# Kernel tuning notes

Measured on AMD Instinct MI355X. Metric: run time of the kernel, lower is better.

## Reference

```python
import jax, jax.numpy as jnp
import numpy as np

L_SIDE = 32
N_PIX = 12 * L_SIDE * L_SIDE      # 12288 sphere pixels
N_VALID = N_PIX // 2              # theta <= pi/2 hemisphere (first half by construction)
A_TH, B_TH, C_TH = 0.03, 1.0, 1.0  # ellipsoid semi-axes (thickness, 1, 1)


def _sphere_angles(n):
    # Deterministic Fibonacci-lattice sphere sampling standing in for SphereHealpix.
    i = np.arange(n, dtype=np.float64)
    z = 1.0 - 2.0 * (i + 0.5) / n          # cos(theta), descending -> theta<=pi/2 iff i < n/2
    theta = np.arccos(z)
    phi = (i * np.pi * (3.0 - np.sqrt(5.0))) % (2.0 * np.pi)
    return theta.astype(np.float32), phi.astype(np.float32)


def _ellipse_valid():
    # Faithful translation of ReconstructionModel.ellipse_valid for the valid hemisphere.
    theta_all, phi_all = _sphere_angles(N_PIX)
    tv = theta_all[:N_VALID].astype(np.float32)
    pv = phi_all[:N_VALID].astype(np.float32)
    a, b, c = np.float32(A_TH), np.float32(B_TH), np.float32(C_TH)
    # cartesian coords of valid pixels (computed BEFORE the angle shift)
    xv = np.cos(pv) * np.sin(tv)
    yv = np.sin(pv) * np.sin(tv)
    # meshgrid(phi, x) / meshgrid(theta, y) with ij indexing -> angles vary on rows, coords on cols
    phi = ((pv + np.pi / 2) % (2 * np.pi)).astype(np.float32)[:, None]   # [Nv,1]
    theta = ((tv + np.pi / 2) % np.pi).astype(np.float32)[:, None]       # [Nv,1]
    x = xv[None, :]
    y = yv[None, :]
    x_c = np.sin(2 * theta) / 2 * np.cos(phi)
    y_c = -np.sin(2 * theta) / 2 * np.sin(phi)
    z_c = (np.cos(2 * theta) + 1) / 2
    r = np.sqrt(2 * (np.cos(2 * theta) + 1)) / 2 + np.float32(1e-5)
    a2, b2, c2 = a * a, b * b, c * c
    ct, st = np.cos(theta), np.sin(theta)
    cp, sp = np.cos(phi), np.sin(phi)
    ct2, ct4 = ct ** 2, ct ** 4
    cp2 = cp ** 2
    x2, y2 = x ** 2, y ** 2
    s2p = np.sin(2.0 * phi)
    with np.errstate(invalid='ignore'):
        S = (-b2 * ct2 + b2 * ct4 - b2 * y2 - c2 * x2
             + a2 * b2 * ct4 + b2 * c2 * ct2 - b2 * c2 * ct4
             - b2 * x2 * cp2 + b2 * y2 * cp2 + c2 * x2 * cp2 - c2 * y2 * cp2
             - a2 * x2 * ct2 + c2 * x2 * ct2
             + b2 * x * y * s2p - c2 * x * y * s2p
             + a2 * x2 * cp2 * ct2 - a2 * y2 * cp2 * ct2
             - c2 * x2 * cp2 * ct2 + c2 * y2 * cp2 * ct2
             + 2.0 * b2 * x * cp * ct * st - 2.0 * b2 * y * ct * sp * st
             + 2.0 * c2 * x * y * cp * ct2 * sp - 2.0 * a2 * x * y * cp * ct2 * sp)
        num = (a * c * np.sqrt(S)
               - a2 * b * ct2 + 2.0 * a2 * b * ct4
               + 2.0 * b * c2 * ct2 - 2.0 * b * c2 * ct4
               + a2 * b * x * cp * ct * st - b * c2 * x * cp * ct * st
               - a2 * b * y * ct * sp * st + b * c2 * y * ct * sp * st)
        den = b * (a2 * ct2 - c2 * ct2 + c2)
        z = num / den
        f = ((x - x_c) ** 2 + (y - y_c) ** 2 + (z - z_c) ** 2) / r ** 2
    f = np.where(np.isnan(f), np.float32(0.0), f)   # f[f != f] = 0
    return f.astype(np.float32)


def setup_inputs() -> dict:
    key = jax.random.key(0)
    x = jax.random.uniform(key, (8, 16, N_PIX), dtype=jnp.float32)
    all_responses = jnp.asarray(_ellipse_valid())   # [N_VALID, N_VALID]
    return {"x": x, "all_responses": all_responses}


def reference(x, all_responses):
    nv = all_responses.shape[0]
    # masked gather: theta <= pi/2 is exactly the first nv pixels by construction
    x_valid = x[:, :, :nv]                                   # [B,C,Nv]
    mixture = jnp.einsum('bcn,nm->bcm', x_valid, all_responses)
    mixture = jnp.clip(mixture, 0.0, 1.0)                    # mix='clip'
    # masked scatter back into zero buffer
    out = jnp.zeros_like(x).at[:, :, :nv].set(mixture)
    return out
```

## Files before the change

kernel.cpp:

```cpp
#include <hip/hip_runtime.h>
#include <hip/hip_bf16.h>


#define NPIX 12288
#define NV   6144
#define MR   128
#define BNW  32
#define KST  128
#define KCH  3072
#define NSI  24

typedef __attribute__((ext_vector_type(8))) short bf16x8;
typedef __attribute__((ext_vector_type(4))) float f32x4;
typedef __attribute__((ext_vector_type(4))) unsigned u32x4;

__device__ __forceinline__ unsigned pk2(float lo, float hi) {
    __hip_bfloat162 h = __float22bfloat162_rn(make_float2(lo, hi));
    union { __hip_bfloat162 h; unsigned u; } v; v.h = h; return v.u;
}

__device__ __forceinline__ bf16x8 cvt8(f32x4 a, f32x4 b) {
    union { unsigned u[4]; bf16x8 v; } r;
    r.u[0] = pk2(a[0], a[1]); r.u[1] = pk2(a[2], a[3]);
    r.u[2] = pk2(b[0], b[1]); r.u[3] = pk2(b[2], b[3]);
    return r.v;
}

__global__ __launch_bounds__(256) void prep_kernel(const float* __restrict__ x,
                                                   unsigned short* __restrict__ abf) {
    int q = blockIdx.x * 256 + threadIdx.x;
    int m = q / (NV / 8);
    int r = q % (NV / 8);
    int k = r * 8;
    const float* src = x + (size_t)m * NPIX + k;
    f32x4 a = *(const f32x4*)(src);
    f32x4 b = *(const f32x4*)(src + 4);
    u32x4 o;
    o[0] = pk2(a[0], a[1]); o[1] = pk2(a[2], a[3]);
    o[2] = pk2(b[0], b[1]); o[3] = pk2(b[2], b[3]);
    *(u32x4*)(abf + (size_t)m * NV + k) = o;
}

__device__ __forceinline__ void sload(const float*& bptr, float2 (&r)[8]) {
    #pragma unroll
    for (int gi = 0; gi < 4; ++gi) {
        const float* p = bptr + (size_t)(gi * 32) * NV;
        r[2 * gi]     = *(const float2*)(p);
        r[2 * gi + 1] = *(const float2*)(p + NV);
    }
    bptr += (size_t)KST * NV;
}

__device__ __forceinline__ void wstage(unsigned char* buf, const float2 (&r)[8],
                                       int kq, int nq, int sw0, int sw1) {
    #pragma unroll
    for (int gi = 0; gi < 4; ++gi) {
        unsigned lo = pk2(r[2 * gi].x, r[2 * gi + 1].x);
        unsigned hi = pk2(r[2 * gi].y, r[2 * gi + 1].y);
        const int kbyte = (kq + gi * 32) * 2;
        *(unsigned*)(buf + nq * 256       + (kbyte ^ sw0)) = lo;
        *(unsigned*)(buf + (nq + 1) * 256 + (kbyte ^ sw1)) = hi;
    }
}

template<bool BF16A>
__device__ __forceinline__ void compute_step(const unsigned char* buf,
        const unsigned short* __restrict__ A, const float* __restrict__ X,
        size_t arow0, size_t arow1, int ln, int lg, f32x4 (&acc)[2][2]) {
    bf16x8 afr[2][4];
    #pragma unroll
    for (int ks = 0; ks < 4; ++ks) {
        if (BF16A) {
            afr[0][ks] = *(const bf16x8*)(A + arow0 + ks * 32);
            afr[1][ks] = *(const bf16x8*)(A + arow1 + ks * 32);
        } else {
            f32x4 p0 = *(const f32x4*)(X + arow0 + ks * 32);
            f32x4 p1 = *(const f32x4*)(X + arow0 + ks * 32 + 4);
            afr[0][ks] = cvt8(p0, p1);
            f32x4 q0 = *(const f32x4*)(X + arow1 + ks * 32);
            f32x4 q1 = *(const f32x4*)(X + arow1 + ks * 32 + 4);
            afr[1][ks] = cvt8(q0, q1);
        }
    }
    const int swn = (ln & 7) << 4;
    #pragma unroll
    for (int nt = 0; nt < 2; ++nt) {
        const int rowb = (nt * 16 + ln) * 256;
        #pragma unroll
        for (int ks = 0; ks < 4; ++ks) {
            bf16x8 bfr = *(const bf16x8*)(buf + rowb + (((lg * 16) + ks * 64) ^ swn));
            acc[0][nt] = __builtin_amdgcn_mfma_f32_16x16x32_bf16(afr[0][ks], bfr, acc[0][nt], 0, 0, 0);
            acc[1][nt] = __builtin_amdgcn_mfma_f32_16x16x32_bf16(afr[1][ks], bfr, acc[1][nt], 0, 0, 0);
        }
    }
}

template<bool BF16A>
__global__ __launch_bounds__(256, 2) void gemm_kernel(const float* __restrict__ X,
        const unsigned short* __restrict__ A, const float* __restrict__ R,
        float* __restrict__ out) {
    __shared__ unsigned char Bs0[32 * 256];
    __shared__ unsigned char Bs1[32 * 256];

    const int tid = threadIdx.x;
    const int w = tid >> 6;
    const int l = tid & 63;
    const int ln = l & 15, lg = l >> 4;
    const int nb = blockIdx.x >> 1, chunk = blockIdx.x & 1;
    const int n0 = nb * BNW;
    const int kbase = chunk * KCH;

    const int kq = (tid >> 4) * 2;
    const int nq = (tid & 15) * 2;
    const float* bptr = R + (size_t)(kbase + kq) * NV + (n0 + nq);
    const int sw0 = (nq & 7) << 4;
    const int sw1 = ((nq + 1) & 7) << 4;

    size_t arow0, arow1;
    if (BF16A) {
        arow0 = (size_t)(w * 32 + ln) * NV + kbase + lg * 8;
        arow1 = arow0 + (size_t)16 * NV;
    } else {
        arow0 = (size_t)(w * 32 + ln) * NPIX + kbase + lg * 8;
        arow1 = arow0 + (size_t)16 * NPIX;
    }

    f32x4 acc[2][2];
    #pragma unroll
    for (int a = 0; a < 2; ++a)
        #pragma unroll
        for (int b = 0; b < 2; ++b) {
            acc[a][b][0] = 0.f; acc[a][b][1] = 0.f;
            acc[a][b][2] = 0.f; acc[a][b][3] = 0.f;
        }

    float2 ring0[8], ring1[8];
    sload(bptr, ring0);
    sload(bptr, ring1);
    wstage(Bs0, ring0, kq, nq, sw0, sw1);
    __syncthreads();

    #pragma unroll 1
    for (int it = 0; it < NSI / 2; ++it) {
        const int s = it * 2;
        if (s + 2 < NSI) sload(bptr, ring0);
        compute_step<BF16A>(Bs0, A, X, arow0, arow1, ln, lg, acc);
        arow0 += KST; arow1 += KST;
        wstage(Bs1, ring1, kq, nq, sw0, sw1);
        __syncthreads();
        if (s + 3 < NSI) sload(bptr, ring1);
        compute_step<BF16A>(Bs1, A, X, arow0, arow1, ln, lg, acc);
        arow0 += KST; arow1 += KST;
        if (s + 2 < NSI) wstage(Bs0, ring0, kq, nq, sw0, sw1);
        __syncthreads();
    }

    #pragma unroll
    for (int mt = 0; mt < 2; ++mt) {
        const int mbase = w * 32 + mt * 16 + lg * 4;
        #pragma unroll
        for (int nt = 0; nt < 2; ++nt) {
            const size_t cb = (size_t)chunk * NV + n0 + nt * 16 + ln;
            #pragma unroll
            for (int j = 0; j < 4; ++j)
                out[(size_t)(mbase + j) * NPIX + cb] = acc[mt][nt][j];
        }
    }
}

__global__ __launch_bounds__(256) void reduce_kernel(float* __restrict__ out) {
    int q = blockIdx.x * 256 + threadIdx.x;
    int m = q / (NV / 4);
    int r = q % (NV / 4);
    size_t base = (size_t)m * NPIX + r * 4;
    f32x4 a = *(f32x4*)(out + base);
    f32x4 b = *(f32x4*)(out + base + NV);
    f32x4 c, z;
    #pragma unroll
    for (int i = 0; i < 4; ++i) {
        float v = a[i] + b[i];
        c[i] = fminf(fmaxf(v, 0.f), 1.f);
        z[i] = 0.f;
    }
    *(f32x4*)(out + base) = c;
    *(f32x4*)(out + base + NV) = z;
}

extern "C" void kernel_launch(void* const* d_in, const int* in_sizes, int n_in,
                              void* d_out, int out_size, void* d_ws, size_t ws_size,
                              hipStream_t stream) {
    const float* x = (const float*)d_in[0];
    const float* R = (const float*)d_in[1];
    float* out = (float*)d_out;

    const bool use_ws = ws_size >= (size_t)MR * NV * 2;
    if (use_ws) {
        unsigned short* abf = (unsigned short*)d_ws;
        prep_kernel<<<(MR * NV / 8) / 256, 256, 0, stream>>>(x, abf);
        gemm_kernel<true><<<(NV / BNW) * 2, 256, 0, stream>>>(x, abf, R, out);
    } else {
        gemm_kernel<false><<<(NV / BNW) * 2, 256, 0, stream>>>(x, nullptr, R, out);
    }
    reduce_kernel<<<(MR * NV / 4) / 256, 256, 0, stream>>>(out);
}
```

Before: 254.4 us.

## Increase split-K chunks to 4 or 8 using workspace partial buffers

Generalizes the split-K GEMM from two K chunks to four or eight, chosen by available workspace. Chunks beyond the first two write partial sums to workspace buffers, and the reduce kernel adds them before clipping. This multiplies the grid from 384 to as many as 1536 blocks so the GPU is better filled. The cost is extra partial-sum writes and reads plus shorter per-block K loops with less pipelining.

```diff
diff --git a/kernel.cpp b/kernel.cpp
--- a/kernel.cpp
+++ b/kernel.cpp
@@ -7,8 +7,8 @@
 #define MR   128
 #define BNW  32
 #define KST  128
-#define KCH  3072
-#define NSI  24
+#define NSTR (NV / BNW)
+#define PARTF ((size_t)MR * NV)
 
 typedef __attribute__((ext_vector_type(8))) short bf16x8;
 typedef __attribute__((ext_vector_type(4))) float f32x4;
@@ -98,7 +98,8 @@
 template<bool BF16A>
 __global__ __launch_bounds__(256, 2) void gemm_kernel(const float* __restrict__ X,
         const unsigned short* __restrict__ A, const float* __restrict__ R,
-        float* __restrict__ out) {
+        float* __restrict__ out, float* __restrict__ wpart,
+        int nchunks, int kch) {
     __shared__ unsigned char Bs0[32 * 256];
     __shared__ unsigned char Bs1[32 * 256];
 
@@ -106,9 +107,11 @@
     const int w = tid >> 6;
     const int l = tid & 63;
     const int ln = l & 15, lg = l >> 4;
-    const int nb = blockIdx.x >> 1, chunk = blockIdx.x & 1;
+    const int chunk = blockIdx.x / NSTR;
+    const int nb = blockIdx.x % NSTR;
     const int n0 = nb * BNW;
-    const int kbase = chunk * KCH;
+    const int kbase = chunk * kch;
+    const int nsi = kch / KST;
 
     const int kq = (tid >> 4) * 2;
     const int nq = (tid & 15) * 2;
@@ -141,48 +144,60 @@
     __syncthreads();
 
     #pragma unroll 1
-    for (int it = 0; it < NSI / 2; ++it) {
+    for (int it = 0; it < nsi / 2; ++it) {
         const int s = it * 2;
-        if (s + 2 < NSI) sload(bptr, ring0);
+        if (s + 2 < nsi) sload(bptr, ring0);
         compute_step<BF16A>(Bs0, A, X, arow0, arow1, ln, lg, acc);
         arow0 += KST; arow1 += KST;
         wstage(Bs1, ring1, kq, nq, sw0, sw1);
         __syncthreads();
-        if (s + 3 < NSI) sload(bptr, ring1);
+        if (s + 3 < nsi) sload(bptr, ring1);
         compute_step<BF16A>(Bs1, A, X, arow0, arow1, ln, lg, acc);
         arow0 += KST; arow1 += KST;
-        if (s + 2 < NSI) wstage(Bs0, ring0, kq, nq, sw0, sw1);
+        if (s + 2 < nsi) wstage(Bs0, ring0, kq, nq, sw0, sw1);
         __syncthreads();
     }
 
+    float* dst;
+    size_t rstride;
+    if (chunk < 2) { dst = out + (size_t)chunk * NV; rstride = NPIX; }
+    else           { dst = wpart + (size_t)(chunk - 2) * PARTF; rstride = NV; }
     #pragma unroll
     for (int mt = 0; mt < 2; ++mt) {
         const int mbase = w * 32 + mt * 16 + lg * 4;
         #pragma unroll
         for (int nt = 0; nt < 2; ++nt) {
-            const size_t cb = (size_t)chunk * NV + n0 + nt * 16 + ln;
+            const size_t cb = (size_t)(n0 + nt * 16 + ln);
             #pragma unroll
             for (int j = 0; j < 4; ++j)
-                out[(size_t)(mbase + j) * NPIX + cb] = acc[mt][nt][j];
-        }
-    }
-}
-
-__global__ __launch_bounds__(256) void reduce_kernel(float* __restrict__ out) {
+                dst[(size_t)(mbase + j) * rstride + cb] = acc[mt][nt][j];
+        }
+    }
+}
+
+__global__ __launch_bounds__(256) void reduce_kernel(float* __restrict__ out,
+        const float* __restrict__ wpart, int nextra) {
     int q = blockIdx.x * 256 + threadIdx.x;
     int m = q / (NV / 4);
     int r = q % (NV / 4);
     size_t base = (size_t)m * NPIX + r * 4;
     f32x4 a = *(f32x4*)(out + base);
     f32x4 b = *(f32x4*)(out + base + NV);
-    f32x4 c, z;
+    #pragma unroll
+    for (int i = 0; i < 4; ++i) a[i] += b[i];
+    #pragma unroll 1
+    for (int p = 0; p < nextra; ++p) {
+        f32x4 c = *(const f32x4*)(wpart + (size_t)p * PARTF + (size_t)m * NV + r * 4);
+        #pragma unroll
+        for (int i = 0; i < 4; ++i) a[i] += c[i];
+    }
+    f32x4 cz, z;
     #pragma unroll
     for (int i = 0; i < 4; ++i) {
-        float v = a[i] + b[i];
-        c[i] = fminf(fmaxf(v, 0.f), 1.f);
+        cz[i] = fminf(fmaxf(a[i], 0.f), 1.f);
         z[i] = 0.f;
     }
-    *(f32x4*)(out + base) = c;
+    *(f32x4*)(out + base) = cz;
     *(f32x4*)(out + base + NV) = z;
 }
 
@@ -193,13 +208,24 @@
     const float* R = (const float*)d_in[1];
     float* out = (float*)d_out;
 
-    const bool use_ws = ws_size >= (size_t)MR * NV * 2;
+    const size_t abytes = (size_t)MR * NV * 2;
+    const bool use_ws = ws_size >= abytes;
+    int chunks = 2;
+    float* wpart = nullptr;
+    if (use_ws) {
+        size_t rem = ws_size - abytes;
+        if      (rem >= 6 * PARTF * 4) chunks = 8;
+        else if (rem >= 2 * PARTF * 4) chunks = 4;
+        wpart = (float*)((char*)d_ws + abytes);
+    }
+    const int kch = NV / chunks;
+
     if (use_ws) {
         unsigned short* abf = (unsigned short*)d_ws;
         prep_kernel<<<(MR * NV / 8) / 256, 256, 0, stream>>>(x, abf);
-        gemm_kernel<true><<<(NV / BNW) * 2, 256, 0, stream>>>(x, abf, R, out);
+        gemm_kernel<true><<<NSTR * chunks, 256, 0, stream>>>(x, abf, R, out, wpart, chunks, kch);
     } else {
-        gemm_kernel<false><<<(NV / BNW) * 2, 256, 0, stream>>>(x, nullptr, R, out);
-    }
-    reduce_kernel<<<(MR * NV / 4) / 256, 256, 0, stream>>>(out);
-}
+        gemm_kernel<false><<<NSTR * chunks, 256, 0, stream>>>(x, nullptr, R, out, wpart, chunks, kch);
+    }
+    reduce_kernel<<<(MR * NV / 4) / 256, 256, 0, stream>>>(out, wpart, chunks - 2);
+}
```

New measurement: 247.8 us. 1.03x faster.
